# Kernel tuning notes

Hardware: AMD Instinct MI355X
Metric: run time of the kernel (lower is better)

Reference implementation:

```python
import jax, jax.numpy as jnp
import numpy as np

B, T, D, H = 2, 512, 512, 8
HD = D // H
FF = 4 * D
MOM_BETA, NOV_BETA, NOV_GAIN = 0.9, 0.95, 3.0
LR_MIN, LR_MAX, MAX_FW_NORM = 0.5, 3.0, 32.0


def setup_inputs() -> dict:
    key = jax.random.key(0)
    ks = jax.random.split(key, 10)
    s = 1.0 / np.sqrt(D)
    return {
        'x': jax.random.normal(ks[0], (B, T, D), jnp.float32),
        'Wq': jax.random.normal(ks[1], (D, D), jnp.float32) * s,
        'Wk1': jax.random.normal(ks[2], (D, D), jnp.float32) * s,
        'Wk2': jax.random.normal(ks[3], (D, D), jnp.float32) * s,
        'Wv': jax.random.normal(ks[4], (D, D), jnp.float32) * s,
        'Wo': jax.random.normal(ks[5], (D, D), jnp.float32) * s,
        'lambda_logit': jnp.zeros((H,), jnp.float32),  # sigmoid -> lambda_init = 0.5
        'ln1_g': jnp.ones((D,), jnp.float32), 'ln1_b': jnp.zeros((D,), jnp.float32),
        'base_weight': jax.random.normal(ks[6], (D, D), jnp.float32) * s,  # ~xavier
        'ttt_bias': jnp.zeros((D,), jnp.float32),
        'log_inner_lr': jnp.log(jnp.asarray(0.05, jnp.float32)),
        'ln2_g': jnp.ones((D,), jnp.float32), 'ln2_b': jnp.zeros((D,), jnp.float32),
        'W1': jax.random.normal(ks[7], (FF, D), jnp.float32) * s,
        'b1': jnp.zeros((FF,), jnp.float32),
        'W2': jax.random.normal(ks[8], (D, FF), jnp.float32) * (1.0 / np.sqrt(FF)),
        'b2': jnp.zeros((D,), jnp.float32),
        'ln3_g': jnp.ones((D,), jnp.float32), 'ln3_b': jnp.zeros((D,), jnp.float32),
    }


def _ln(x, g, b):
    m = x.mean(-1, keepdims=True)
    v = jnp.mean((x - m) ** 2, -1, keepdims=True)
    return (x - m) / jnp.sqrt(v + 1e-5) * g + b


def _diff_attn(x, Wq, Wk1, Wk2, Wv, Wo, lambda_logit):
    b, t, d = x.shape
    def heads(w):
        return jnp.einsum('btd,od->bto', x, w).reshape(b, t, H, HD).transpose(0, 2, 1, 3)
    q, k1, k2, v = heads(Wq), heads(Wk1), heads(Wk2), heads(Wv)
    scale = HD ** -0.5
    s1 = jnp.einsum('bhqd,bhkd->bhqk', q, k1) * scale
    s2 = jnp.einsum('bhqd,bhkd->bhqk', q, k2) * scale
    mask = jnp.tril(jnp.ones((t, t), bool))
    neg = jnp.finfo(s1.dtype).min
    s1 = jnp.where(mask, s1, neg)
    s2 = jnp.where(mask, s2, neg)
    lam = jax.nn.sigmoid(lambda_logit)[None, :, None, None]
    attn = jax.nn.softmax(s1, -1) - lam * jax.nn.softmax(s2, -1)
    attn = attn / jnp.clip(jnp.abs(attn).sum(-1, keepdims=True), 1e-6, None)
    o = jnp.einsum('bhqk,bhkd->bhqd', attn, v).transpose(0, 2, 1, 3).reshape(b, t, d)
    return jnp.einsum('btd,od->bto', o, Wo)


def _ttt(x, base_weight, ttt_bias, log_inner_lr):
    b = x.shape[0]
    inner_lr = jnp.clip(jnp.exp(log_inner_lr), 1e-5, 1.0)
    fw0 = jnp.broadcast_to(base_weight, (b, D, D)).astype(x.dtype) + 0.0
    mom0 = jnp.zeros_like(fw0)
    ema0 = jnp.zeros((b, D), x.dtype)
    lrm0 = jnp.ones((b, 1), x.dtype)

    def step(carry, x_t):  # x_t: [B, D]
        fw, mom, ema, lrm = carry
        y = jnp.einsum('bij,bj->bi', fw, x_t) + ttt_bias
        err = (y - x_t) / float(D)  # targets=None -> target is x_t
        g = jax.lax.stop_gradient(err[:, :, None] * x_t[:, None, :])  # first_order
        mom2 = MOM_BETA * mom + (1.0 - MOM_BETA) * g
        nov = jnp.abs(x_t - ema).mean(-1, keepdims=True)  # [B, 1]
        lr_scale = jnp.clip(1.0 + NOV_GAIN * nov, LR_MIN, LR_MAX)
        lrm2 = NOV_BETA * lrm + (1.0 - NOV_BETA) * lr_scale
        ema2 = NOV_BETA * ema + (1.0 - NOV_BETA) * x_t
        fw2 = fw - (inner_lr * lrm2)[:, :, None] * mom2
        norm = jnp.clip(jnp.sqrt((fw2 * fw2).sum((1, 2), keepdims=True)), 1e-6, None)
        fw2 = fw2 * jnp.minimum(MAX_FW_NORM / norm, 1.0)
        return (fw2, mom2, ema2, lrm2), y

    _, ys = jax.lax.scan(step, (fw0, mom0, ema0, lrm0), x.transpose(1, 0, 2))
    return ys.transpose(1, 0, 2)


def reference(x, Wq, Wk1, Wk2, Wv, Wo, lambda_logit, ln1_g, ln1_b, base_weight, ttt_bias, log_inner_lr, ln2_g, ln2_b, W1, b1, W2, b2, ln3_g, ln3_b):
    h = x + _diff_attn(_ln(x, ln1_g, ln1_b), Wq, Wk1, Wk2, Wv, Wo, lambda_logit)
    h = h + _ttt(_ln(h, ln2_g, ln2_b), base_weight, ttt_bias, log_inner_lr)
    z = _ln(h, ln3_g, ln3_b)
    z = jax.nn.gelu(jnp.einsum('btd,fd->btf', z, W1) + b1, approximate=False)
    h = h + jnp.einsum('btf,df->btd', z, W2) + b2
    return h
```

## Files before the change

kernel.cpp:

```cpp
#include <hip/hip_runtime.h>
#include <hip/hip_fp16.h>

typedef _Float16 f16;
typedef f16 f16x4 __attribute__((ext_vector_type(4)));
typedef f16 f16x8 __attribute__((ext_vector_type(8)));
typedef float f32x4 __attribute__((ext_vector_type(4)));

#define DEVI static __device__ __forceinline__

DEVI void gload_lds16(const void* g, void* l) {
  __builtin_amdgcn_global_load_lds(
      (const __attribute__((address_space(1))) unsigned int*)g,
      (__attribute__((address_space(3))) unsigned int*)l, 16, 0, 0);
}

DEVI float wave_red_sum64(float v) {
#pragma unroll
  for (int m = 1; m < 64; m <<= 1) v += __shfl_xor(v, m, 64);
  return v;
}
DEVI float wave_red_max64(float v) {
#pragma unroll
  for (int m = 1; m < 64; m <<= 1) v = fmaxf(v, __shfl_xor(v, m, 64));
  return v;
}

template <int CTRL>
DEVI float dpp_addf(float v) {
  int s = __builtin_amdgcn_update_dpp(0, __float_as_int(v), CTRL, 0xF, 0xF, true);
  return v + __int_as_float(s);
}
DEVI float redsum64(float v) {
  v = dpp_addf<0xB1>(v);
  v = dpp_addf<0x4E>(v);
  v = dpp_addf<0x141>(v);
  v = dpp_addf<0x140>(v);
  int t = __builtin_amdgcn_update_dpp(0, __float_as_int(v), 0x142, 0xA, 0xF, true);
  v += __int_as_float(t);
  t = __builtin_amdgcn_update_dpp(0, __float_as_int(v), 0x143, 0xC, 0xF, true);
  v += __int_as_float(t);
  return __int_as_float(__builtin_amdgcn_readlane(__float_as_int(v), 63));
}

__global__ void cvt_all_kernel(const float* __restrict__ s0, const float* __restrict__ s1,
                               const float* __restrict__ s2, const float* __restrict__ s3,
                               const float* __restrict__ s4, const float* __restrict__ s5,
                               const float* __restrict__ s6, f16* __restrict__ d,
                               const float* __restrict__ x, const float* __restrict__ ln1g,
                               const float* __restrict__ ln1b, f16* __restrict__ xlnH) {
  const int blk = blockIdx.x;
  if (blk >= 3328) {
    const int row = (blk - 3328) * 4 + ((int)threadIdx.x >> 6);
    const int lane = threadIdx.x & 63;
    const long base = (long)row * 512;
    const int c0 = lane * 4, c1 = 256 + lane * 4;
    float4 a0 = *(const float4*)(x + base + c0);
    float4 a1 = *(const float4*)(x + base + c1);
    float v[8] = {a0.x, a0.y, a0.z, a0.w, a1.x, a1.y, a1.z, a1.w};
    float s = 0.f;
#pragma unroll
    for (int k = 0; k < 8; k++) s += v[k];
    s = wave_red_sum64(s);
    const float mean = s * (1.f / 512.f);
    float vs = 0.f;
#pragma unroll
    for (int k = 0; k < 8; k++) { float dd = v[k] - mean; vs += dd * dd; }
    vs = wave_red_sum64(vs);
    const float rstd = rsqrtf(vs * (1.f / 512.f) + 1e-5f);
    float4 g0 = *(const float4*)(ln1g + c0), g1 = *(const float4*)(ln1g + c1);
    float4 p0 = *(const float4*)(ln1b + c0), p1 = *(const float4*)(ln1b + c1);
    const float gg[8] = {g0.x, g0.y, g0.z, g0.w, g1.x, g1.y, g1.z, g1.w};
    const float bv[8] = {p0.x, p0.y, p0.z, p0.w, p1.x, p1.y, p1.z, p1.w};
    float y[8];
#pragma unroll
    for (int k = 0; k < 8; k++) y[k] = (v[k] - mean) * rstd * gg[k] + bv[k];
    f16x4 o0 = {(f16)y[0], (f16)y[1], (f16)y[2], (f16)y[3]};
    f16x4 o1 = {(f16)y[4], (f16)y[5], (f16)y[6], (f16)y[7]};
    *(f16x4*)(xlnH + base + c0) = o0;
    *(f16x4*)(xlnH + base + c1) = o1;
    return;
  }
  const float* s; long dofs; int local;
  if (blk < 256)       { s = s0; dofs = 0;       local = blk; }
  else if (blk < 512)  { s = s1; dofs = 262144;  local = blk - 256; }
  else if (blk < 768)  { s = s2; dofs = 524288;  local = blk - 512; }
  else if (blk < 1024) { s = s3; dofs = 786432;  local = blk - 768; }
  else if (blk < 1280) { s = s4; dofs = 1048576; local = blk - 1024; }
  else if (blk < 2304) { s = s5; dofs = 1310720; local = blk - 1280; }
  else                 { s = s6; dofs = 2359296; local = blk - 2304; }
  const long i = (long)local * 1024 + threadIdx.x * 4;
  float4 v = *(const float4*)(s + i);
  f16x4 o = {(f16)v.x, (f16)v.y, (f16)v.z, (f16)v.w};
  *(f16x4*)(d + dofs + i) = o;
}

__global__ void ln_kernel(const float* __restrict__ in, const float* __restrict__ add,
                          const float* __restrict__ g, const float* __restrict__ b,
                          float* __restrict__ sumout, float* __restrict__ lnf,
                          f16* __restrict__ lnh) {
  const int row = blockIdx.x * 4 + (threadIdx.x >> 6);
  const int lane = threadIdx.x & 63;
  const long base = (long)row * 512;
  const int c0 = lane * 4, c1 = 256 + lane * 4;
  float4 a0 = *(const float4*)(in + base + c0);
  float4 a1 = *(const float4*)(in + base + c1);
  if (add) {
    float4 d0 = *(const float4*)(add + base + c0);
    float4 d1 = *(const float4*)(add + base + c1);
    a0.x += d0.x; a0.y += d0.y; a0.z += d0.z; a0.w += d0.w;
    a1.x += d1.x; a1.y += d1.y; a1.z += d1.z; a1.w += d1.w;
  }
  if (sumout) {
// ... 3 lines not shown
  float v[8] = {a0.x, a0.y, a0.z, a0.w, a1.x, a1.y, a1.z, a1.w};
  float s = 0.f;
#pragma unroll
  for (int k = 0; k < 8; k++) s += v[k];
  s = wave_red_sum64(s);
  const float mean = s * (1.f / 512.f);
  float vs = 0.f;
#pragma unroll
  for (int k = 0; k < 8; k++) { float d = v[k] - mean; vs += d * d; }
  vs = wave_red_sum64(vs);
  const float rstd = rsqrtf(vs * (1.f / 512.f) + 1e-5f);
  float4 g0 = *(const float4*)(g + c0), g1 = *(const float4*)(g + c1);
  float4 p0 = *(const float4*)(b + c0), p1 = *(const float4*)(b + c1);
  const float gg[8] = {g0.x, g0.y, g0.z, g0.w, g1.x, g1.y, g1.z, g1.w};
  const float bv[8] = {p0.x, p0.y, p0.z, p0.w, p1.x, p1.y, p1.z, p1.w};
  float y[8];
#pragma unroll
  for (int k = 0; k < 8; k++) y[k] = (v[k] - mean) * rstd * gg[k] + bv[k];
  if (lnf) {
    float4 o0 = {y[0], y[1], y[2], y[3]}, o1 = {y[4], y[5], y[6], y[7]};
    *(float4*)(lnf + base + c0) = o0;
    *(float4*)(lnf + base + c1) = o1;
  }
  if (lnh) {
    f16x4 o0 = {(f16)y[0], (f16)y[1], (f16)y[2], (f16)y[3]};
    f16x4 o1 = {(f16)y[4], (f16)y[5], (f16)y[6], (f16)y[7]};
    *(f16x4*)(lnh + base + c0) = o0;
    *(f16x4*)(lnh + base + c1) = o1;
  }
}

__global__ void red8ln_kernel(const float* __restrict__ parts, const float* __restrict__ xres,
                              const float* __restrict__ g, const float* __restrict__ b,
                              float* __restrict__ h1, float* __restrict__ x2out) {
  const int row = blockIdx.x * 4 + (threadIdx.x >> 6);
  const int lane = threadIdx.x & 63;
  const long base = (long)row * 512;
  const int c0 = lane * 4, c1 = 256 + lane * 4;
  float4 a0, a1;
  {
    float4 r = *(const float4*)(xres + base + c0);
    float sx = r.x, sy = r.y, sz = r.z, sw = r.w;
#pragma unroll
    for (int sl = 0; sl < 8; sl++) {
      float4 p = *(const float4*)(parts + (long)sl * 524288 + base + c0);
      sx += p.x; sy += p.y; sz += p.z; sw += p.w;
    }
    a0 = (float4){sx, sy, sz, sw};
  }
  {
    float4 r = *(const float4*)(xres + base + c1);
    float sx = r.x, sy = r.y, sz = r.z, sw = r.w;
#pragma unroll
    for (int sl = 0; sl < 8; sl++) {
      float4 p = *(const float4*)(parts + (long)sl * 524288 + base + c1);
      sx += p.x; sy += p.y; sz += p.z; sw += p.w;
    }
    a1 = (float4){sx, sy, sz, sw};
  }
  *(float4*)(h1 + base + c0) = a0;
  *(float4*)(h1 + base + c1) = a1;
  float v[8] = {a0.x, a0.y, a0.z, a0.w, a1.x, a1.y, a1.z, a1.w};
  float s = 0.f;
#pragma unroll
  for (int k = 0; k < 8; k++) s += v[k];
  s = wave_red_sum64(s);
  const float mean = s * (1.f / 512.f);
  float vs = 0.f;
#pragma unroll
  for (int k = 0; k < 8; k++) { float d = v[k] - mean; vs += d * d; }
  vs = wave_red_sum64(vs);
  const float rstd = rsqrtf(vs * (1.f / 512.f) + 1e-5f);
  float4 g0 = *(const float4*)(g + c0), g1 = *(const float4*)(g + c1);
  float4 p0 = *(const float4*)(b + c0), p1 = *(const float4*)(b + c1);
  const float gg[8] = {g0.x, g0.y, g0.z, g0.w, g1.x, g1.y, g1.z, g1.w};
  const float bv[8] = {p0.x, p0.y, p0.z, p0.w, p1.x, p1.y, p1.z, p1.w};
  float y[8];
#pragma unroll
  for (int k = 0; k < 8; k++) y[k] = (v[k] - mean) * rstd * gg[k] + bv[k];
  float4 o0 = {y[0], y[1], y[2], y[3]}, o1 = {y[4], y[5], y[6], y[7]};
  *(float4*)(x2out + base + c0) = o0;
  *(float4*)(x2out + base + c1) = o1;
}

enum { EPI_SCORES = 2, EPI_PV = 3, EPI_PART = 7, EPI_QKVPART = 8, EPI_GPART = 9 };

template <int EPI>
__launch_bounds__(256, 1) __global__
void gemm_bt(const f16* __restrict__ A, const f16* __restrict__ W, int lda, int ldw,
             long Az, long Wz, void* __restrict__ dst, const float* __restrict__ bias,
             const float* __restrict__ resid, int K, float scale, int zofs, int hcp) {
  if (EPI == EPI_SCORES && blockIdx.x > blockIdx.y) return;
  __shared__ f16 lA[128 * 64];
  __shared__ f16 lB[128 * 64];
  const int tid = threadIdx.x;
  const int wave = tid >> 6, lane = tid & 63;
  const int z = blockIdx.z;
  const f16* Ab;
  const f16* Wb;
  if (EPI == EPI_SCORES) {
    const int v_ = (z >= hcp) ? 1 : 0, head = z - v_ * hcp;
    Ab = A + (long)head * 32768 + (long)blockIdx.y * 128 * lda;
    Wb = W + (long)v_ * 524288 + (long)head * 32768 + (long)blockIdx.x * 128 * ldw;
  } else if (EPI == EPI_QKVPART) {
    const int widx = z & 3, ks = z >> 2;
    Ab = A + (long)blockIdx.y * 128 * lda + (long)ks * Az;
    Wb = W + (long)widx * Wz + (long)blockIdx.x * 128 * ldw + (long)ks * Az;
  } else {
    Ab = A + (long)z * Az + (long)blockIdx.y * 128 * lda;
    Wb = W + (long)z * Wz + (long)blockIdx.x * 128 * ldw;
  }

  f32x4 acc[4][4];
#pragma unroll
  for (int a = 0; a < 4; a++)
#pragma unroll
    for (int q = 0; q < 4; q++) acc[a][q] = (f32x4){0.f, 0.f, 0.f, 0.f};

// ... 30 lines not shown
      for (int nf = 0; nf < 4; nf++) {
        int r = wn + nf * 16 + (lane & 15);
        bfv[nf] = *(const f16x8*)((const char*)lB + r * 128 + (kb ^ ((r & 7) << 4)));
      }
#pragma unroll
      for (int mf = 0; mf < 4; mf++)
#pragma unroll
        for (int nf = 0; nf < 4; nf++)
          acc[mf][nf] = __builtin_amdgcn_mfma_f32_16x16x32_f16(af[mf], bfv[nf], acc[mf][nf], 0, 0, 0);
    }
  }

  const int wm = (wave >> 1) * 64, wn = (wave & 1) * 64;
  const int rbase = blockIdx.y * 128 + wm + ((lane >> 4) << 2);
  const int cbase = blockIdx.x * 128 + wn + (lane & 15);
#pragma unroll
  for (int mf = 0; mf < 4; mf++)
#pragma unroll
    for (int nf = 0; nf < 4; nf++)
#pragma unroll
      for (int j = 0; j < 4; j++) {
        const int m = rbase + mf * 16 + j;
        const int n = cbase + nf * 16;
        const float v = acc[mf][nf][j];
        if (EPI == EPI_SCORES) {
          ((float*)dst)[(long)z * 262144 + (long)m * 512 + n] = v * scale;
        } else if (EPI == EPI_PV) {
          if (n < 64) {
            const int hh = z + zofs;
            ((f16*)dst)[(long)((hh >> 3) * 512 + m) * 512 + (hh & 7) * 64 + n] = (f16)v;
          }
        } else if (EPI == EPI_GPART) {
          ((float*)dst)[(long)z * 2097152 + (long)m * 2048 + n] = v;
        } else {
          ((float*)dst)[(long)z * 524288 + (long)m * 512 + n] = v;
        }
      }
}

__global__ void qkv_red_kernel(const float* __restrict__ parts, f16* __restrict__ qkv) {
  const int idx = blockIdx.x * 256 + threadIdx.x;
  const int w = idx >> 17;
  const int r = idx & 131071;
  const int m = r >> 7;
  const int n4 = (r & 127) << 2;
  const float* p0 = parts + (long)w * 524288 + (long)m * 512 + n4;
  float4 a = *(const float4*)p0;
  float4 b = *(const float4*)(p0 + 4l * 524288);
  const float s0 = a.x + b.x, s1 = a.y + b.y, s2 = a.z + b.z, s3 = a.w + b.w;
  const int mb = (m >> 9) * 8 + (n4 >> 6);
  if (w < 3) {
    f16* d = qkv + (long)w * 524288;
    f16x4 o = {(f16)s0, (f16)s1, (f16)s2, (f16)s3};
    *(f16x4*)(d + (long)mb * 32768 + (m & 511) * 64 + (n4 & 63)) = o;
  } else {
    f16* d = qkv + 3l * 524288;
    const long bb = (long)mb * 32768 + (m & 511);
    d[bb + (long)(n4 & 63) * 512]       = (f16)s0;
    d[bb + (long)((n4 & 63) + 1) * 512] = (f16)s1;
    d[bb + (long)((n4 & 63) + 2) * 512] = (f16)s2;
    d[bb + (long)((n4 & 63) + 3) * 512] = (f16)s3;
  }
}

__global__ void red2gelu_kernel(const float* __restrict__ parts, const float* __restrict__ bias,
                                f16* __restrict__ zh) {
// ... 43 lines not shown
  float s1v[8] = {xa.x, xa.y, xa.z, xa.w, xb.x, xb.y, xb.z, xb.w};
  float s2v[8] = {ya.x, ya.y, ya.z, ya.w, yb.x, yb.y, yb.z, yb.w};
  int cols[8];
#pragma unroll
  for (int k = 0; k < 8; k++) cols[k] = (k < 4) ? (c0 + k) : (c1 + k - 4);
  float m1 = -3.0e38f, m2 = -3.0e38f;
#pragma unroll
  for (int k = 0; k < 8; k++)
    if (cols[k] <= i) { m1 = fmaxf(m1, s1v[k]); m2 = fmaxf(m2, s2v[k]); }
  m1 = wave_red_max64(m1);
  m2 = wave_red_max64(m2);
  float z1 = 0.f, z2 = 0.f, e1[8], e2[8];
#pragma unroll
  for (int k = 0; k < 8; k++) {
    const bool valid = cols[k] <= i;
    e1[k] = valid ? __expf(s1v[k] - m1) : 0.f;
    e2[k] = valid ? __expf(s2v[k] - m2) : 0.f;
    z1 += e1[k]; z2 += e2[k];
  }
  z1 = wave_red_sum64(z1);
  z2 = wave_red_sum64(z2);
  const float r1 = 1.f / z1, r2 = lam / z2;
  float p[8], l1 = 0.f;
#pragma unroll
  for (int k = 0; k < 8; k++) { p[k] = e1[k] * r1 - e2[k] * r2; l1 += fabsf(p[k]); }
  l1 = wave_red_sum64(l1);
  const float rn = 1.f / fmaxf(l1, 1e-6f);
  f16x4 o0 = {(f16)(p[0] * rn), (f16)(p[1] * rn), (f16)(p[2] * rn), (f16)(p[3] * rn)};
  f16x4 o1 = {(f16)(p[4] * rn), (f16)(p[5] * rn), (f16)(p[6] * rn), (f16)(p[7] * rn)};
  *(f16x4*)(attn + base + c0) = o0;
  *(f16x4*)(attn + base + c1) = o1;
}

#define ALD4(dst, p) asm volatile("global_load_dwordx4 %0, %1, off" : "=&v"(dst) : "v"(p) : "memory")
#define ALD1(dst, p) asm volatile("global_load_dword %0, %1, off" : "=&v"(dst) : "v"(p) : "memory")
#define VMWAIT(N)                                                             \
  {                                                                           \
    asm volatile("s_waitcnt vmcnt(" #N ")" ::: "memory");                     \
    __builtin_amdgcn_sched_barrier(0);                                        \
  }

#define EISSUE(X)                                                             \
  {                                                                           \
    ALD1(X[0], pe);        ALD1(X[1], pe + 512);                              \
    ALD1(X[2], pe + 1024); ALD1(X[3], pe + 1536);                             \
    ALD1(X[4], pe + 2048); ALD1(X[5], pe + 2560);                             \
    ALD1(X[6], pe + 3072); ALD1(X[7], pe + 3584);                             \
    pe += 4096;                                                               \
  }
#define ESTEP(V, T)                                                           \
  {                                                                           \
    dp[(long)(T) * 512] = fabsf((V) - ema);                                   \
    ema = fmaf(0.95f, ema, 0.05f * (V));                                      \
  }

__launch_bounds__(64, 1) __global__
void eta_diff_kernel(const float* __restrict__ x2, float* __restrict__ diff) {
  const int blk = blockIdx.x;
  const int b = blk >> 3;
  const int col = (blk & 7) * 64 + threadIdx.x;
  const float* pe = x2 + (long)b * 262144 + col;
  float* dp = diff + (long)b * 262144 + col;
  float ema = 0.f;
  float EA[8], EB[8];
  EISSUE(EA);
  EISSUE(EB);
  VMWAIT(8);
// ... 10 lines not shown
  }
  asm volatile("s_waitcnt vmcnt(0)" ::: "memory");
}

__global__ void eta_nov_kernel(const float* __restrict__ diff, float* __restrict__ nov,
                               int* __restrict__ flag) {
  if (blockIdx.x == 0 && threadIdx.x == 0) flag[0] = 0;
  const int row = blockIdx.x * 4 + (threadIdx.x >> 6);
  const int lane = threadIdx.x & 63;
  const float* dp = diff + (long)row * 512 + lane * 4;
  float4 a0 = *(const float4*)dp;
  float4 a1 = *(const float4*)(dp + 256);
  float s = ((a0.x + a0.y) + (a0.z + a0.w)) + ((a1.x + a1.y) + (a1.z + a1.w));
  s = wave_red_sum64(s);
  if (lane == 0) nov[row] = s * (1.f / 512.f);
}

__global__ void eta_scan_kernel(const float* __restrict__ nov, const float* __restrict__ loglr,
                                float* __restrict__ eta) {
  if (threadIdx.x != 0) return;
  const int b = blockIdx.x;
  float ilr = expf(loglr[0]);
  ilr = fminf(fmaxf(ilr, 1e-5f), 1.f);
  float lrm = 1.f;
  const float* pb = nov + (long)b * 512;
#pragma unroll 8
  for (int t = 0; t < 512; t++) {
    const float ls = fminf(fmaxf(fmaf(3.f, pb[t], 1.f), 0.5f), 3.f);
    lrm = fmaf(0.95f, lrm, 0.05f * ls);
    eta[b * 512 + t] = ilr * lrm;
  }
}

DEVI float dot8(const f32x4 F0, const f32x4 F1, const f32x4 X0, const f32x4 X1) {
  float a0 = F0.x * X0.x, a1 = F0.y * X0.y, a2 = F0.z * X0.z, a3 = F0.w * X0.w;
  a0 = fmaf(F1.x, X1.x, a0); a1 = fmaf(F1.y, X1.y, a1);
  a2 = fmaf(F1.z, X1.z, a2); a3 = fmaf(F1.w, X1.w, a3);
  return (a0 + a1) + (a2 + a3);
}
DEVI void upd8(f32x4& M0, f32x4& M1, f32x4& F0, f32x4& F1, float c1, float e,
               const f32x4 X0, const f32x4 X1, float& ns) {
  M0.x = fmaf(0.9f, M0.x, c1 * X0.x); F0.x = fmaf(-e, M0.x, F0.x); ns = fmaf(F0.x, F0.x, ns);
  M0.y = fmaf(0.9f, M0.y, c1 * X0.y); F0.y = fmaf(-e, M0.y, F0.y); ns = fmaf(F0.y, F0.y, ns);
  M0.z = fmaf(0.9f, M0.z, c1 * X0.z); F0.z = fmaf(-e, M0.z, F0.z); ns = fmaf(F0.z, F0.z, ns);
  M0.w = fmaf(0.9f, M0.w, c1 * X0.w); F0.w = fmaf(-e, M0.w, F0.w); ns = fmaf(F0.w, F0.w, ns);
  M1.x = fmaf(0.9f, M1.x, c1 * X1.x); F1.x = fmaf(-e, M1.x, F1.x); ns = fmaf(F1.x, F1.x, ns);
  M1.y = fmaf(0.9f, M1.y, c1 * X1.y); F1.y = fmaf(-e, M1.y, F1.y); ns = fmaf(F1.y, F1.y, ns);
  M1.z = fmaf(0.9f, M1.z, c1 * X1.z); F1.z = fmaf(-e, M1.z, F1.z); ns = fmaf(F1.z, F1.z, ns);
  M1.w = fmaf(0.9f, M1.w, c1 * X1.w); F1.w = fmaf(-e, M1.w, F1.w); ns = fmaf(F1.w, F1.w, ns);
}

#define TISSUE2(X, RA, RB, ET)                                                \
  {                                                                           \
    ALD4(X[0], pxc);        ALD4(X[1], pxc + 4);                              \
    ALD4(X[2], pxc + 512);  ALD4(X[3], pxc + 516);                            \
    ALD4(X[4], pxc + 1024); ALD4(X[5], pxc + 1028);                           \
    ALD4(X[6], pxc + 1536); ALD4(X[7], pxc + 1540);                           \
    ALD1(RA[0], pxra);        ALD1(RA[1], pxra + 512);                        \
    ALD1(RA[2], pxra + 1024); ALD1(RA[3], pxra + 1536);                       \
    ALD1(RB[0], pxrb);        ALD1(RB[1], pxrb + 512);                        \
    ALD1(RB[2], pxrb + 1024); ALD1(RB[3], pxrb + 1536);                       \
    ALD4(ET, per);                                                            \
    pxc += 2048; pxra += 2048; pxrb += 2048; per += 4;                        \
  }

#define TSTEP2(X0v, X1v, rAv, rBv, ev, K)                                     \
  {                                                                           \
    const float pA_ = redsum64(dot8(fA0, fA1, X0v, X1v));                     \
    const float pB_ = redsum64(dot8(fB0, fB1, X0v, X1v));                     \
    const float yA_ = pA_ + biasA, yB_ = pB_ + biasB;                         \
    ysA[K] = yA_; ysB[K] = yB_;                                               \
    const float c1A_ = (yA_ - (rAv)) * (0.1f / 512.f);                        \
    const float c1B_ = (yB_ - (rBv)) * (0.1f / 512.f);                        \
    const float e_ = (ev);                                                    \
    float ns_ = 0.f;                                                          \
    upd8(mA0, mA1, fA0, fA1, c1A_, e_, X0v, X1v, ns_);                        \
    upd8(mB0, mB1, fB0, fB1, c1B_, e_, X0v, X1v, ns_);                        \
    nsmax = fmaxf(nsmax, ns_);                                                \
  }

__launch_bounds__(64, 1) __global__
void ttt_fast_kernel(const float* __restrict__ x2, const float* __restrict__ base_w,
                     const float* __restrict__ tbias, const float* __restrict__ eta,
                     float* __restrict__ yT, float* __restrict__ npB) {
  const int blk = blockIdx.x;
  const int b = blk >> 8;
  const int rA = blk & 255;
  const int lane = threadIdx.x;
  const float* xb = x2 + (long)b * 262144;

  f32x4 fA0, fA1, fB0, fB1;
  float biasA, biasB;
  ALD4(fA0, base_w + (long)rA * 512 + lane * 8);
  ALD4(fA1, base_w + (long)rA * 512 + lane * 8 + 4);
  ALD4(fB0, base_w + (long)(rA + 256) * 512 + lane * 8);
  ALD4(fB1, base_w + (long)(rA + 256) * 512 + lane * 8 + 4);
  ALD1(biasA, tbias + rA);
  ALD1(biasB, tbias + rA + 256);

  f32x4 mA0 = {0.f, 0.f, 0.f, 0.f}, mA1 = mA0, mB0 = mA0, mB1 = mA0;
  float ysA[8], ysB[8];
  float nsmax = 0.f;

  const float* pxc = xb + lane * 8;
  const float* pxra = xb + rA;
  const float* pxrb = xb + rA + 256;
  const float* per = eta + b * 512;
  float* pyA = yT + (long)(b * 512 + rA) * 512;
  float* pyB = yT + (long)(b * 512 + rA + 256) * 512;

  f32x4 XA[8], XB[8], EA, EB;
  float RA0[4], RB0[4], RA1[4], RB1[4];
  TISSUE2(XA, RA0, RB0, EA);
  TISSUE2(XB, RA1, RB1, EB);
  VMWAIT(17);

#pragma unroll 1
  for (int T = 0; T < 512; T += 8) {
    TSTEP2(XA[0], XA[1], RA0[0], RB0[0], EA.x, 0);
    TSTEP2(XA[2], XA[3], RA0[1], RB0[1], EA.y, 1);
    TSTEP2(XA[4], XA[5], RA0[2], RB0[2], EA.z, 2);
    TSTEP2(XA[6], XA[7], RA0[3], RB0[3], EA.w, 3);
    TISSUE2(XA, RA0, RB0, EA);
    VMWAIT(17);
    TSTEP2(XB[0], XB[1], RA1[0], RB1[0], EB.x, 4);
    TSTEP2(XB[2], XB[3], RA1[1], RB1[1], EB.y, 5);
    TSTEP2(XB[4], XB[5], RA1[2], RB1[2], EB.z, 6);
    TSTEP2(XB[6], XB[7], RA1[3], RB1[3], EB.w, 7);
    if (lane == 0) {
      *(float4*)(pyA + T)     = (float4){ysA[0], ysA[1], ysA[2], ysA[3]};
      *(float4*)(pyA + T + 4) = (float4){ysA[4], ysA[5], ysA[6], ysA[7]};
      *(float4*)(pyB + T)     = (float4){ysB[0], ysB[1], ysB[2], ysB[3]};
      *(float4*)(pyB + T + 4) = (float4){ysB[4], ysB[5], ysB[6], ysB[7]};
    }
    TISSUE2(XB, RA1, RB1, EB);
    VMWAIT(21);
  }
  asm volatile("s_waitcnt vmcnt(0)" ::: "memory");
  const float tot = redsum64(nsmax);
  if (lane == 0) npB[blk] = tot;
}

__global__ void transpose2v_kernel(const float* __restrict__ yT, float* __restrict__ ysb,
                                   const float* __restrict__ npB, int* __restrict__ flag) {
  const int s = blockIdx.z;
  if (s == 2) {
    if (blockIdx.x != 0 || blockIdx.y != 0) return;
    const int tid = threadIdx.x;
    const int wave = tid >> 6, lane = tid & 63;
    float a = npB[tid];
    float c = npB[tid + 256];
    a = wave_red_sum64(a);
    c = wave_red_sum64(c);
    __shared__ float pa[4], pc[4];
    if (lane == 0) { pa[wave] = a; pc[wave] = c; }
    __syncthreads();
    if (tid == 0) {
      const float s0 = (pa[0] + pa[1]) + (pa[2] + pa[3]);
      const float s1 = (pc[0] + pc[1]) + (pc[2] + pc[3]);
      if (s0 > 1000.f || s1 > 1000.f) atomicOr(flag, 1);
    }
    return;
  }
  __shared__ float tile[64][65];
  const float* src = yT + (long)s * 262144;
  float* dst = ysb + (long)s * 262144;
  const int ti = blockIdx.y, tj = blockIdx.x;
  const int tr = threadIdx.x >> 4;
  const int tc = (threadIdx.x & 15) * 4;
#pragma unroll
  for (int p = 0; p < 4; p++) {
    const int r = tr + p * 16;
    float4 v = *(const float4*)(src + (long)(ti * 64 + r) * 512 + tj * 64 + tc);
    tile[r][tc] = v.x; tile[r][tc + 1] = v.y; tile[r][tc + 2] = v.z; tile[r][tc + 3] = v.w;
  }
  __syncthreads();
#pragma unroll
  for (int p = 0; p < 4; p++) {
    const int j = tr + p * 16;
    float4 v = {tile[tc][j], tile[tc + 1][j], tile[tc + 2][j], tile[tc + 3][j]};
    *(float4*)(dst + (long)(tj * 64 + j) * 512 + ti * 64 + tc) = v;
  }
}

__launch_bounds__(1024, 1) __global__
void ttt_fallback_kernel(const int* __restrict__ flag, const float* __restrict__ x2,
                         const float* __restrict__ base_w, const float* __restrict__ tbias,
                         const float* __restrict__ eta, float* __restrict__ ys,
                         float* __restrict__ fwg, float* __restrict__ momg) {
  if (flag[0] == 0) return;
  const int b = blockIdx.x;
  const int tid = threadIdx.x;
  const int wave = tid >> 6, lane = tid & 63;
  float* fw = fwg + (long)b * 262144;
  float* mm = momg + (long)b * 262144;
  for (int e = tid; e < 262144; e += 1024) { fw[e] = base_w[e]; mm[e] = 0.f; }
  __shared__ float xs[512], errs[512], red[16];
  const float* xb = x2 + (long)b * 262144;
  for (int t = 0; t < 512; t++) {
    __syncthreads();
    if (tid < 512) xs[tid] = xb[t * 512 + tid];
    __syncthreads();
    if (tid < 512) {
      float acc = 0.f;
      for (int c = 0; c < 512; c++) acc = fmaf(fw[(long)tid * 512 + c], xs[c], acc);
      const float y = acc + tbias[tid];
      ys[((long)b * 512 + t) * 512 + tid] = y;
      errs[tid] = (y - xs[tid]) * (1.f / 512.f);
    }
    __syncthreads();
    const float eta_t = eta[b * 512 + t];
    float nsq = 0.f;
    for (int e = tid; e < 262144; e += 1024) {
      const int r = e >> 9, c = e & 511;
      const float m2 = fmaf(0.9f, mm[e], 0.1f * errs[r] * xs[c]);
// ... 38 lines not shown
  const float* ln2b   = (const float*)d_in[13];
  const float* W1     = (const float*)d_in[14];
  const float* b1     = (const float*)d_in[15];
  const float* W2     = (const float*)d_in[16];
  const float* b2     = (const float*)d_in[17];
  const float* ln3g   = (const float*)d_in[18];
  const float* ln3b   = (const float*)d_in[19];
  float* out = (float*)d_out;

  char* ws = (char*)d_ws;
  size_t off = 0;
  auto alloc = [&](size_t bytes) {
    size_t o = off;
    off += (bytes + 255) & ~(size_t)255;
    return o;
  };
  f16* WqH   = (f16*)(ws + alloc(262144 * 2));
  f16* Wk1H  = (f16*)(ws + alloc(262144 * 2));
  f16* Wk2H  = (f16*)(ws + alloc(262144 * 2));
  f16* WvH   = (f16*)(ws + alloc(262144 * 2));
  f16* WoH   = (f16*)(ws + alloc(262144 * 2));
  f16* W1H   = (f16*)(ws + alloc(1048576 * 2));
  f16* W2H   = (f16*)(ws + alloc(1048576 * 2));
  (void)Wk1H; (void)Wk2H; (void)WvH; (void)W1H;
  f16* xlnH  = (f16*)(ws + alloc(524288 * 2));
  f16* qh    = (f16*)(ws + alloc(524288 * 2));
  f16* k1h   = (f16*)(ws + alloc(524288 * 2));
  f16* k2h   = (f16*)(ws + alloc(524288 * 2));
  f16* vTh   = (f16*)(ws + alloc(524288 * 2));
  (void)k2h;
  f16* obtd  = (f16*)(ws + alloc(524288 * 2));
  f16* x3h   = (f16*)(ws + alloc(524288 * 2));
  f16* zh    = (f16*)(ws + alloc(2097152 * 2));
  float* h1  = (float*)(ws + alloc(524288 * 4));
  float* x2  = (float*)(ws + alloc(524288 * 4));
  float* ysb = (float*)(ws + alloc(524288 * 4));
  float* h2  = (float*)(ws + alloc(524288 * 4));
  float* eta = (float*)(ws + alloc(1024 * 4));
  float* npB = (float*)(ws + alloc(512 * 4));
  float* nov = (float*)(ws + alloc(1024 * 4));
  int* flag  = (int*)(ws + alloc(256));
  float* parts16 = (float*)(ws + alloc((size_t)16 * 1024 * 1024));
  float* yT    = parts16;
  float* nvd   = parts16 + 524288;
  float* fwfb  = parts16 + 1048576;
  float* momfb = parts16 + 1572864;

  int hc = 16;
  while (hc > 1 && off + (size_t)hc * (262144ull * 4 * 2 + 262144ull * 2) > ws_size) hc >>= 1;
  float* S1  = (float*)(ws + alloc((size_t)hc * 262144 * 4));
  float* S2  = (float*)(ws + alloc((size_t)hc * 262144 * 4));
  f16* attnb = (f16*)(ws + alloc((size_t)hc * 262144 * 2));
  (void)S2;

  cvt_all_kernel<<<3584, 256, 0, stream>>>(Wq, Wk1, Wk2, Wv, Wo, W1, W2, WqH,
                                           x, ln1g, ln1b, xlnH);

  gemm_bt<EPI_QKVPART><<<dim3(4, 8, 8), 256, 0, stream>>>(
      xlnH, WqH, 512, 512, 256, 262144, parts16, nullptr, nullptr, 256, 1.f, 0, 0);
  qkv_red_kernel<<<2048, 256, 0, stream>>>(parts16, qh);

  const int nc = 16 / hc;
  for (int c = 0; c < nc; c++) {
    const int cs = c * hc;
    gemm_bt<EPI_SCORES><<<dim3(4, 4, 2 * hc), 256, 0, stream>>>(
        qh + (long)cs * 32768, k1h + (long)cs * 32768, 64, 64, 0, 0, S1,
        nullptr, nullptr, 64, 0.125f, 0, hc);
    softmax_diff_kernel<<<hc * 128, 256, 0, stream>>>(S1, S2, lamlog, attnb, cs);
    gemm_bt<EPI_PV><<<dim3(1, 4, hc), 256, 0, stream>>>(
        attnb, vTh + (long)cs * 32768, 512, 512, 262144, 32768, obtd,
        nullptr, nullptr, 512, 1.f, cs, 0);
  }

  gemm_bt<EPI_PART><<<dim3(4, 8, 8), 256, 0, stream>>>(
      obtd, WoH, 512, 512, 64, 64, parts16, nullptr, nullptr, 64, 1.f, 0, 0);
  red8ln_kernel<<<256, 256, 0, stream>>>(parts16, x, ln2g, ln2b, h1, x2);

  eta_diff_kernel<<<16, 64, 0, stream>>>(x2, nvd);
  eta_nov_kernel<<<256, 256, 0, stream>>>(nvd, nov, flag);
  eta_scan_kernel<<<2, 64, 0, stream>>>(nov, loglr, eta);
  ttt_fast_kernel<<<512, 64, 0, stream>>>(x2, basew, tttb, eta, yT, npB);
  transpose2v_kernel<<<dim3(8, 8, 3), 256, 0, stream>>>(yT, ysb, npB, flag);
  ttt_fallback_kernel<<<2, 1024, 0, stream>>>(flag, x2, basew, tttb, eta, ysb, fwfb, momfb);

  ln_kernel<<<256, 256, 0, stream>>>(h1, ysb, ln3g, ln3b, h2, nullptr, x3h);

  gemm_bt<EPI_GPART><<<dim3(16, 8, 2), 256, 0, stream>>>(
      x3h, W1H, 512, 512, 256, 256, parts16, nullptr, nullptr, 256, 1.f, 0, 0);
  red2gelu_kernel<<<2048, 256, 0, stream>>>(parts16, b1, zh);
  gemm_bt<EPI_PART><<<dim3(4, 8, 8), 256, 0, stream>>>(
      zh, W2H, 2048, 2048, 256, 256, parts16, nullptr, nullptr, 256, 1.f, 0, 0);
  red8_kernel<<<512, 256, 0, stream>>>(parts16, h2, b2, out);
}
```

Measured before the change: 273.3 us.

## Replace sequential TTT scan with Gram-matrix triangular solve formulation

Drops the per-token sequential fast-weight recurrence kernel. In its place, the TTT outputs are rewritten algebraically: x2·base_weightᵀ and the Gram matrix x2·x2ᵀ come from fp16 GEMMs, a per-batch table of momentum-weighted learning rates is built, and a blocked lower-triangular solve recovers the per-token errors. The fast-weight norm check is rebuilt from further GEMMs and reductions, and the original fallback kernel still runs when the norm clip would trigger. Long serial dependency chains become mostly matrix work. The price is fp16 rounding in the Gram and error terms and a solve kernel that runs on only 16 blocks.

```diff
diff --git a/kernel.cpp b/kernel.cpp
--- a/kernel.cpp
+++ b/kernel.cpp
@@ -25,32 +25,16 @@
   return v;
 }
 
-template <int CTRL>
-DEVI float dpp_addf(float v) {
-  int s = __builtin_amdgcn_update_dpp(0, __float_as_int(v), CTRL, 0xF, 0xF, true);
-  return v + __int_as_float(s);
-}
-DEVI float redsum64(float v) {
-  v = dpp_addf<0xB1>(v);
-  v = dpp_addf<0x4E>(v);
-  v = dpp_addf<0x141>(v);
-  v = dpp_addf<0x140>(v);
-  int t = __builtin_amdgcn_update_dpp(0, __float_as_int(v), 0x142, 0xA, 0xF, true);
-  v += __int_as_float(t);
-  t = __builtin_amdgcn_update_dpp(0, __float_as_int(v), 0x143, 0xC, 0xF, true);
-  v += __int_as_float(t);
-  return __int_as_float(__builtin_amdgcn_readlane(__float_as_int(v), 63));
-}
-
 __global__ void cvt_all_kernel(const float* __restrict__ s0, const float* __restrict__ s1,
                                const float* __restrict__ s2, const float* __restrict__ s3,
                                const float* __restrict__ s4, const float* __restrict__ s5,
                                const float* __restrict__ s6, f16* __restrict__ d,
+                               const float* __restrict__ bw, f16* __restrict__ bwh,
                                const float* __restrict__ x, const float* __restrict__ ln1g,
                                const float* __restrict__ ln1b, f16* __restrict__ xlnH) {
   const int blk = blockIdx.x;
-  if (blk >= 3328) {
-    const int row = (blk - 3328) * 4 + ((int)threadIdx.x >> 6);
+  if (blk >= 3584) {
+    const int row = (blk - 3584) * 4 + ((int)threadIdx.x >> 6);
     const int lane = threadIdx.x & 63;
     const long base = (long)row * 512;
     const int c0 = lane * 4, c1 = 256 + lane * 4;
@@ -78,6 +62,13 @@
     f16x4 o1 = {(f16)y[4], (f16)y[5], (f16)y[6], (f16)y[7]};
     *(f16x4*)(xlnH + base + c0) = o0;
     *(f16x4*)(xlnH + base + c1) = o1;
+    return;
+  }
+  if (blk >= 3328) {
+    const long i = (long)(blk - 3328) * 1024 + threadIdx.x * 4;
+    float4 v = *(const float4*)(bw + i);
+    f16x4 o = {(f16)v.x, (f16)v.y, (f16)v.z, (f16)v.w};
+    *(f16x4*)(bwh + i) = o;
     return;
   }
   const float* s; long dofs; int local;
@@ -147,7 +138,8 @@
 
 __global__ void red8ln_kernel(const float* __restrict__ parts, const float* __restrict__ xres,
                               const float* __restrict__ g, const float* __restrict__ b,
-                              float* __restrict__ h1, float* __restrict__ x2out) {
+                              float* __restrict__ h1, float* __restrict__ x2out,
+                              f16* __restrict__ x2h) {
   const int row = blockIdx.x * 4 + (threadIdx.x >> 6);
   const int lane = threadIdx.x & 63;
   const long base = (long)row * 512;
@@ -196,9 +188,14 @@
   float4 o0 = {y[0], y[1], y[2], y[3]}, o1 = {y[4], y[5], y[6], y[7]};
   *(float4*)(x2out + base + c0) = o0;
   *(float4*)(x2out + base + c1) = o1;
-}
-
-enum { EPI_SCORES = 2, EPI_PV = 3, EPI_PART = 7, EPI_QKVPART = 8, EPI_GPART = 9 };
+  f16x4 h0 = {(f16)y[0], (f16)y[1], (f16)y[2], (f16)y[3]};
+  f16x4 hh1 = {(f16)y[4], (f16)y[5], (f16)y[6], (f16)y[7]};
+  *(f16x4*)(x2h + base + c0) = h0;
+  *(f16x4*)(x2h + base + c1) = hh1;
+}
+
+enum { EPI_SCORES = 2, EPI_PV = 3, EPI_PART = 7, EPI_QKVPART = 8, EPI_GPART = 9,
+       EPI_GRAM = 10, EPI_MXG = 11 };
 
 template <int EPI>
 __launch_bounds__(256, 1) __global__
@@ -295,6 +292,11 @@
           }
         } else if (EPI == EPI_GPART) {
           ((float*)dst)[(long)z * 2097152 + (long)m * 2048 + n] = v;
+        } else if (EPI == EPI_GRAM) {
+          ((float*)dst)[(long)z * 262144 + (long)m * 512 + n] = v * scale;
+        } else if (EPI == EPI_MXG) {
+          const long ii = (long)z * 262144 + (long)m * 512 + n;
+          ((f16*)dst)[ii] = (f16)(v * resid[ii] * (1.f / 262144.f));
         } else {
           ((float*)dst)[(long)z * 524288 + (long)m * 512 + n] = v;
         }
@@ -404,7 +406,6 @@
   *(f16x4*)(attn + base + c1) = o1;
 }
 
-#define ALD4(dst, p) asm volatile("global_load_dwordx4 %0, %1, off" : "=&v"(dst) : "v"(p) : "memory")
 #define ALD1(dst, p) asm volatile("global_load_dword %0, %1, off" : "=&v"(dst) : "v"(p) : "memory")
 #define VMWAIT(N)                                                             \
   {                                                                           \
@@ -481,155 +482,153 @@
   }
 }
 
-DEVI float dot8(const f32x4 F0, const f32x4 F1, const f32x4 X0, const f32x4 X1) {
-  float a0 = F0.x * X0.x, a1 = F0.y * X0.y, a2 = F0.z * X0.z, a3 = F0.w * X0.w;
-  a0 = fmaf(F1.x, X1.x, a0); a1 = fmaf(F1.y, X1.y, a1);
-  a2 = fmaf(F1.z, X1.z, a2); a3 = fmaf(F1.w, X1.w, a3);
-  return (a0 + a1) + (a2 + a3);
-}
-DEVI void upd8(f32x4& M0, f32x4& M1, f32x4& F0, f32x4& F1, float c1, float e,
-               const f32x4 X0, const f32x4 X1, float& ns) {
-  M0.x = fmaf(0.9f, M0.x, c1 * X0.x); F0.x = fmaf(-e, M0.x, F0.x); ns = fmaf(F0.x, F0.x, ns);
-  M0.y = fmaf(0.9f, M0.y, c1 * X0.y); F0.y = fmaf(-e, M0.y, F0.y); ns = fmaf(F0.y, F0.y, ns);
-  M0.z = fmaf(0.9f, M0.z, c1 * X0.z); F0.z = fmaf(-e, M0.z, F0.z); ns = fmaf(F0.z, F0.z, ns);
-  M0.w = fmaf(0.9f, M0.w, c1 * X0.w); F0.w = fmaf(-e, M0.w, F0.w); ns = fmaf(F0.w, F0.w, ns);
-  M1.x = fmaf(0.9f, M1.x, c1 * X1.x); F1.x = fmaf(-e, M1.x, F1.x); ns = fmaf(F1.x, F1.x, ns);
-  M1.y = fmaf(0.9f, M1.y, c1 * X1.y); F1.y = fmaf(-e, M1.y, F1.y); ns = fmaf(F1.y, F1.y, ns);
-  M1.z = fmaf(0.9f, M1.z, c1 * X1.z); F1.z = fmaf(-e, M1.z, F1.z); ns = fmaf(F1.z, F1.z, ns);
-  M1.w = fmaf(0.9f, M1.w, c1 * X1.w); F1.w = fmaf(-e, M1.w, F1.w); ns = fmaf(F1.w, F1.w, ns);
-}
-
-#define TISSUE2(X, RA, RB, ET)                                                \
-  {                                                                           \
-    ALD4(X[0], pxc);        ALD4(X[1], pxc + 4);                              \
-    ALD4(X[2], pxc + 512);  ALD4(X[3], pxc + 516);                            \
-    ALD4(X[4], pxc + 1024); ALD4(X[5], pxc + 1028);                           \
-    ALD4(X[6], pxc + 1536); ALD4(X[7], pxc + 1540);                           \
-    ALD1(RA[0], pxra);        ALD1(RA[1], pxra + 512);                        \
-    ALD1(RA[2], pxra + 1024); ALD1(RA[3], pxra + 1536);                       \
-    ALD1(RB[0], pxrb);        ALD1(RB[1], pxrb + 512);                        \
-    ALD1(RB[2], pxrb + 1024); ALD1(RB[3], pxrb + 1536);                       \
-    ALD4(ET, per);                                                            \
-    pxc += 2048; pxra += 2048; pxrb += 2048; per += 4;                        \
-  }
-
-#define TSTEP2(X0v, X1v, rAv, rBv, ev, K)                                     \
-  {                                                                           \
-    const float pA_ = redsum64(dot8(fA0, fA1, X0v, X1v));                     \
-    const float pB_ = redsum64(dot8(fB0, fB1, X0v, X1v));                     \
-    const float yA_ = pA_ + biasA, yB_ = pB_ + biasB;                         \
-    ysA[K] = yA_; ysB[K] = yB_;                                               \
-    const float c1A_ = (yA_ - (rAv)) * (0.1f / 512.f);                        \
-    const float c1B_ = (yB_ - (rBv)) * (0.1f / 512.f);                        \
-    const float e_ = (ev);                                                    \
-    float ns_ = 0.f;                                                          \
-    upd8(mA0, mA1, fA0, fA1, c1A_, e_, X0v, X1v, ns_);                        \
-    upd8(mB0, mB1, fB0, fB1, c1B_, e_, X0v, X1v, ns_);                        \
-    nsmax = fmaxf(nsmax, ns_);                                                \
-  }
-
-__launch_bounds__(64, 1) __global__
-void ttt_fast_kernel(const float* __restrict__ x2, const float* __restrict__ base_w,
-                     const float* __restrict__ tbias, const float* __restrict__ eta,
-                     float* __restrict__ yT, float* __restrict__ npB) {
-  const int blk = blockIdx.x;
-  const int b = blk >> 8;
-  const int rA = blk & 255;
-  const int lane = threadIdx.x;
-  const float* xb = x2 + (long)b * 262144;
-
-  f32x4 fA0, fA1, fB0, fB1;
-  float biasA, biasB;
-  ALD4(fA0, base_w + (long)rA * 512 + lane * 8);
-  ALD4(fA1, base_w + (long)rA * 512 + lane * 8 + 4);
-  ALD4(fB0, base_w + (long)(rA + 256) * 512 + lane * 8);
-  ALD4(fB1, base_w + (long)(rA + 256) * 512 + lane * 8 + 4);
-  ALD1(biasA, tbias + rA);
-  ALD1(biasB, tbias + rA + 256);
-
-  f32x4 mA0 = {0.f, 0.f, 0.f, 0.f}, mA1 = mA0, mB0 = mA0, mB1 = mA0;
-  float ysA[8], ysB[8];
-  float nsmax = 0.f;
-
-  const float* pxc = xb + lane * 8;
-  const float* pxra = xb + rA;
-  const float* pxrb = xb + rA + 256;
-  const float* per = eta + b * 512;
-  float* pyA = yT + (long)(b * 512 + rA) * 512;
-  float* pyB = yT + (long)(b * 512 + rA + 256) * 512;
-
-  f32x4 XA[8], XB[8], EA, EB;
-  float RA0[4], RB0[4], RA1[4], RB1[4];
-  TISSUE2(XA, RA0, RB0, EA);
-  TISSUE2(XB, RA1, RB1, EB);
-  VMWAIT(17);
-
-#pragma unroll 1
-  for (int T = 0; T < 512; T += 8) {
-    TSTEP2(XA[0], XA[1], RA0[0], RB0[0], EA.x, 0);
-    TSTEP2(XA[2], XA[3], RA0[1], RB0[1], EA.y, 1);
-    TSTEP2(XA[4], XA[5], RA0[2], RB0[2], EA.z, 2);
-    TSTEP2(XA[6], XA[7], RA0[3], RB0[3], EA.w, 3);
-    TISSUE2(XA, RA0, RB0, EA);
-    VMWAIT(17);
-    TSTEP2(XB[0], XB[1], RA1[0], RB1[0], EB.x, 4);
-    TSTEP2(XB[2], XB[3], RA1[1], RB1[1], EB.y, 5);
-    TSTEP2(XB[4], XB[5], RA1[2], RB1[2], EB.z, 6);
-    TSTEP2(XB[6], XB[7], RA1[3], RB1[3], EB.w, 7);
-    if (lane == 0) {
-      *(float4*)(pyA + T)     = (float4){ysA[0], ysA[1], ysA[2], ysA[3]};
-      *(float4*)(pyA + T + 4) = (float4){ysA[4], ysA[5], ysA[6], ysA[7]};
-      *(float4*)(pyB + T)     = (float4){ysB[0], ysB[1], ysB[2], ysB[3]};
-      *(float4*)(pyB + T + 4) = (float4){ysB[4], ysB[5], ysB[6], ysB[7]};
-    }
-    TISSUE2(XB, RA1, RB1, EB);
-    VMWAIT(21);
-  }
-  asm volatile("s_waitcnt vmcnt(0)" ::: "memory");
-  const float tot = redsum64(nsmax);
-  if (lane == 0) npB[blk] = tot;
-}
-
-__global__ void transpose2v_kernel(const float* __restrict__ yT, float* __restrict__ ysb,
-                                   const float* __restrict__ npB, int* __restrict__ flag) {
-  const int s = blockIdx.z;
-  if (s == 2) {
-    if (blockIdx.x != 0 || blockIdx.y != 0) return;
-    const int tid = threadIdx.x;
-    const int wave = tid >> 6, lane = tid & 63;
-    float a = npB[tid];
-    float c = npB[tid + 256];
-    a = wave_red_sum64(a);
-    c = wave_red_sum64(c);
-    __shared__ float pa[4], pc[4];
-    if (lane == 0) { pa[wave] = a; pc[wave] = c; }
-    __syncthreads();
-    if (tid == 0) {
-      const float s0 = (pa[0] + pa[1]) + (pa[2] + pa[3]);
-      const float s1 = (pc[0] + pc[1]) + (pc[2] + pc[3]);
-      if (s0 > 1000.f || s1 > 1000.f) atomicOr(flag, 1);
-    }
+__global__ void wtab_kernel(const float* __restrict__ eta, const float* __restrict__ basew,
+                            float* __restrict__ wUT32, f16* __restrict__ wUT16,
+                            float* __restrict__ fwn2) {
+  if (blockIdx.x == 2) {
+    __shared__ float part[512];
+    float s = 0.f;
+    for (int e = threadIdx.x; e < 262144; e += 512) { float v = basew[e]; s = fmaf(v, v, s); }
+    part[threadIdx.x] = s;
+    __syncthreads();
+    for (int st = 256; st > 0; st >>= 1) {
+      if ((int)threadIdx.x < st) part[threadIdx.x] += part[threadIdx.x + st];
+      __syncthreads();
+    }
+    if (threadIdx.x == 0) fwn2[0] = part[0];
     return;
   }
-  __shared__ float tile[64][65];
-  const float* src = yT + (long)s * 262144;
-  float* dst = ysb + (long)s * 262144;
-  const int ti = blockIdx.y, tj = blockIdx.x;
-  const int tr = threadIdx.x >> 4;
-  const int tc = (threadIdx.x & 15) * 4;
-#pragma unroll
-  for (int p = 0; p < 4; p++) {
-    const int r = tr + p * 16;
-    float4 v = *(const float4*)(src + (long)(ti * 64 + r) * 512 + tj * 64 + tc);
-    tile[r][tc] = v.x; tile[r][tc + 1] = v.y; tile[r][tc + 2] = v.z; tile[r][tc + 3] = v.w;
-  }
-  __syncthreads();
-#pragma unroll
-  for (int p = 0; p < 4; p++) {
-    const int j = tr + p * 16;
-    float4 v = {tile[tc][j], tile[tc + 1][j], tile[tc + 2][j], tile[tc + 3][j]};
-    *(float4*)(dst + (long)(tj * 64 + j) * 512 + ti * 64 + tc) = v;
-  }
+  const int b = blockIdx.x, u = threadIdx.x;
+  const float* et = eta + b * 512;
+  float* w32 = wUT32 + (long)b * 262144;
+  f16* w16 = wUT16 + (long)b * 262144;
+  float q = 0.1f, wv = 0.f;
+  for (int t = 0; t < 512; t++) {
+    if (t < u) {
+      w32[(long)t * 512 + u] = 0.f;
+      w16[(long)t * 512 + u] = (f16)0.f;
+    } else {
+      wv = fmaf(q, et[t], wv);
+      q *= 0.9f;
+      w32[(long)t * 512 + u] = wv;
+      w16[(long)t * 512 + u] = (f16)wv;
+    }
+  }
+}
+
+__global__ void e0_kernel(const float* __restrict__ Y0, const float* __restrict__ x2,
+                          const float* __restrict__ tttb, float* __restrict__ e0) {
+  const long i = ((long)blockIdx.x * 256 + threadIdx.x) * 4;
+  float4 y = *(const float4*)(Y0 + i);
+  float4 x = *(const float4*)(x2 + i);
+  float4 bb = *(const float4*)(tttb + (int)(i & 511));
+  float4 o = {(y.x + bb.x - x.x) * (1.f / 512.f), (y.y + bb.y - x.y) * (1.f / 512.f),
+              (y.z + bb.z - x.z) * (1.f / 512.f), (y.w + bb.w - x.w) * (1.f / 512.f)};
+  *(float4*)(e0 + i) = o;
+}
+
+__global__ void solve_kernel(const float* __restrict__ e0, const float* __restrict__ wUT32,
+                             const float* __restrict__ G, const float* __restrict__ x2,
+                             float* __restrict__ E, f16* __restrict__ Eh,
+                             float* __restrict__ ysb) {
+  extern __shared__ char smem[];
+  f16* Elds = (f16*)smem;
+  float* Ls = (float*)(smem + 65536);
+  float* Rhs = (float*)(smem + 65536 + 16384);
+  const int b = blockIdx.z, g = blockIdx.x;
+  const int tid = threadIdx.x, w = tid >> 6, l = tid & 63;
+  const int c = g * 64 + l;
+  const float* e0b = e0 + (long)b * 262144;
+  const float* wb = wUT32 + (long)b * 262144;
+  const float* Gb = G + (long)b * 262144;
+  const float* x2b = x2 + (long)b * 262144;
+  float* Eb = E + (long)b * 262144;
+  f16* Ehb = Eh + (long)b * 262144;
+  float* ysp = ysb + (long)b * 262144;
+
+  for (int i = 0; i < 8; i++) {
+    const int t0 = i * 64;
+    float acc[8];
+#pragma unroll
+    for (int r = 0; r < 8; r++) acc[r] = e0b[(long)(t0 + w * 8 + r) * 512 + c];
+    for (int j = 0; j < i; j++) {
+      __syncthreads();
+      for (int e = tid; e < 4096; e += 512) {
+        const int tp = e >> 6, up = e & 63;
+        Ls[e] = wb[(long)(t0 + tp - 1) * 512 + j * 64 + up] *
+                Gb[(long)(t0 + tp) * 512 + j * 64 + up] * (1.f / 512.f);
+      }
+      __syncthreads();
+      for (int up = 0; up < 64; up++) {
+        const float ev = (float)Elds[(j * 64 + up) * 64 + l];
+#pragma unroll
+        for (int r = 0; r < 8; r++)
+          acc[r] = fmaf(-Ls[(w * 8 + r) * 64 + up], ev, acc[r]);
+      }
+    }
+    __syncthreads();
+#pragma unroll
+    for (int r = 0; r < 8; r++) Rhs[(w * 8 + r) * 64 + l] = acc[r];
+    for (int e = tid; e < 4096; e += 512) {
+      const int tp = e >> 6, up = e & 63;
+      if (up < tp)
+        Ls[e] = wb[(long)(t0 + tp - 1) * 512 + i * 64 + up] *
+                Gb[(long)(t0 + tp) * 512 + i * 64 + up] * (1.f / 512.f);
+    }
+    __syncthreads();
+    if (w == 0) {
+      float ech[64];
+#pragma unroll
+      for (int tp = 0; tp < 64; tp++) {
+        float v = Rhs[tp * 64 + l];
+#pragma unroll
+        for (int up = 0; up < tp; up++)
+          v = fmaf(-Ls[tp * 64 + up], ech[up], v);
+        ech[tp] = v;
+        Elds[(t0 + tp) * 64 + l] = (f16)v;
+      }
+#pragma unroll
+      for (int tp = 0; tp < 64; tp++) {
+        const long gi = (long)(t0 + tp) * 512 + c;
+        const float v = ech[tp];
+        Eb[gi] = v;
+        Ehb[gi] = (f16)(512.f * v);
+        ysp[gi] = fmaf(512.f, v, x2b[gi]);
+      }
+    }
+    __syncthreads();
+  }
+}
+
+__global__ void a_kernel(const float* __restrict__ E, const float* __restrict__ Y0,
+                         float* __restrict__ a) {
+  const int row = blockIdx.x * 4 + (threadIdx.x >> 6);
+  const int lane = threadIdx.x & 63;
+  const float* ep = E + (long)row * 512 + lane * 4;
+  const float* yp = Y0 + (long)row * 512 + lane * 4;
+  float4 e0v = *(const float4*)ep, y0 = *(const float4*)yp;
+  float4 e1 = *(const float4*)(ep + 256), y1 = *(const float4*)(yp + 256);
+  float s = ((e0v.x * y0.x + e0v.y * y0.y) + (e0v.z * y0.z + e0v.w * y0.w)) +
+            ((e1.x * y1.x + e1.y * y1.y) + (e1.z * y1.z + e1.w * y1.w));
+  s = wave_red_sum64(s);
+  if (lane == 0) a[row] = s;
+}
+
+__global__ void normt_kernel(const float* __restrict__ wUT32, const float* __restrict__ V,
+                             const float* __restrict__ a, const float* __restrict__ fwn2,
+                             int* __restrict__ flag) {
+  const int b = blockIdx.x, t = threadIdx.x;
+  const float* wrow = wUT32 + (long)b * 262144 + (long)t * 512;
+  const float* ab = a + b * 512;
+  const float* Vb = V + (long)b * 262144;
+  float s1 = 0.f, s2 = 0.f;
+  for (int u = 0; u <= t; u++) {
+    const float wv = wrow[u];
+    s1 = fmaf(wv, ab[u], s1);
+    s2 = fmaf(wv, Vb[(long)u * 512 + t], s2);
+  }
+  const float n2 = fwn2[0] - 2.f * s1 + s2;
+  if (n2 > 1000.f) atomicOr(flag, 1);
 }
 
 __launch_bounds__(1024, 1) __global__
@@ -734,19 +733,30 @@
   f16* obtd  = (f16*)(ws + alloc(524288 * 2));
   f16* x3h   = (f16*)(ws + alloc(524288 * 2));
   f16* zh    = (f16*)(ws + alloc(2097152 * 2));
+  f16* x2h   = (f16*)(ws + alloc(524288 * 2));
+  f16* bwh   = (f16*)(ws + alloc(262144 * 2));
   float* h1  = (float*)(ws + alloc(524288 * 4));
   float* x2  = (float*)(ws + alloc(524288 * 4));
   float* ysb = (float*)(ws + alloc(524288 * 4));
   float* h2  = (float*)(ws + alloc(524288 * 4));
   float* eta = (float*)(ws + alloc(1024 * 4));
-  float* npB = (float*)(ws + alloc(512 * 4));
   float* nov = (float*)(ws + alloc(1024 * 4));
   int* flag  = (int*)(ws + alloc(256));
   float* parts16 = (float*)(ws + alloc((size_t)16 * 1024 * 1024));
-  float* yT    = parts16;
-  float* nvd   = parts16 + 524288;
-  float* fwfb  = parts16 + 1048576;
-  float* momfb = parts16 + 1572864;
+  float* Y0    = parts16;
+  float* Gg    = parts16 + 524288;
+  float* wUT32 = parts16 + 1048576;
+  float* e0b   = parts16 + 1572864;
+  float* Ebuf  = parts16 + 2097152;
+  float* nvd   = parts16 + 2621440;
+  float* Vb    = nvd;
+  f16* wUT16   = (f16*)(parts16 + 3145728);
+  f16* Ehb     = (f16*)(parts16 + 3407872);
+  f16* Mxh     = (f16*)(parts16 + 3670016);
+  float* ab    = parts16 + 3932160;
+  float* fwn2  = parts16 + 3933184;
+  float* fwfb  = Y0;
+  float* momfb = Gg;
 
   int hc = 16;
   while (hc > 1 && off + (size_t)hc * (262144ull * 4 * 2 + 262144ull * 2) > ws_size) hc >>= 1;
@@ -755,8 +765,8 @@
   f16* attnb = (f16*)(ws + alloc((size_t)hc * 262144 * 2));
   (void)S2;
 
-  cvt_all_kernel<<<3584, 256, 0, stream>>>(Wq, Wk1, Wk2, Wv, Wo, W1, W2, WqH,
-                                           x, ln1g, ln1b, xlnH);
+  cvt_all_kernel<<<3840, 256, 0, stream>>>(Wq, Wk1, Wk2, Wv, Wo, W1, W2, WqH,
+                                           basew, bwh, x, ln1g, ln1b, xlnH);
 
   gemm_bt<EPI_QKVPART><<<dim3(4, 8, 8), 256, 0, stream>>>(
       xlnH, WqH, 512, 512, 256, 262144, parts16, nullptr, nullptr, 256, 1.f, 0, 0);
@@ -776,13 +786,24 @@
 
   gemm_bt<EPI_PART><<<dim3(4, 8, 8), 256, 0, stream>>>(
       obtd, WoH, 512, 512, 64, 64, parts16, nullptr, nullptr, 64, 1.f, 0, 0);
-  red8ln_kernel<<<256, 256, 0, stream>>>(parts16, x, ln2g, ln2b, h1, x2);
-
+  red8ln_kernel<<<256, 256, 0, stream>>>(parts16, x, ln2g, ln2b, h1, x2, x2h);
+
+  gemm_bt<EPI_GRAM><<<dim3(4, 4, 2), 256, 0, stream>>>(
+      x2h, bwh, 512, 512, 262144, 0, Y0, nullptr, nullptr, 512, 1.f, 0, 0);
+  gemm_bt<EPI_GRAM><<<dim3(4, 4, 2), 256, 0, stream>>>(
+      x2h, x2h, 512, 512, 262144, 262144, Gg, nullptr, nullptr, 512, 1.f, 0, 0);
   eta_diff_kernel<<<16, 64, 0, stream>>>(x2, nvd);
   eta_nov_kernel<<<256, 256, 0, stream>>>(nvd, nov, flag);
   eta_scan_kernel<<<2, 64, 0, stream>>>(nov, loglr, eta);
-  ttt_fast_kernel<<<512, 64, 0, stream>>>(x2, basew, tttb, eta, yT, npB);
-  transpose2v_kernel<<<dim3(8, 8, 3), 256, 0, stream>>>(yT, ysb, npB, flag);
+  wtab_kernel<<<3, 512, 0, stream>>>(eta, basew, wUT32, wUT16, fwn2);
+  e0_kernel<<<512, 256, 0, stream>>>(Y0, x2, tttb, e0b);
+  solve_kernel<<<dim3(8, 1, 2), 512, 98304, stream>>>(e0b, wUT32, Gg, x2, Ebuf, Ehb, ysb);
+  gemm_bt<EPI_MXG><<<dim3(4, 4, 2), 256, 0, stream>>>(
+      Ehb, Ehb, 512, 512, 262144, 262144, Mxh, nullptr, Gg, 512, 1.f, 0, 0);
+  gemm_bt<EPI_GRAM><<<dim3(4, 4, 2), 256, 0, stream>>>(
+      Mxh, wUT16, 512, 512, 262144, 262144, Vb, nullptr, nullptr, 512, 1.f, 0, 0);
+  a_kernel<<<256, 256, 0, stream>>>(Ebuf, Y0, ab);
+  normt_kernel<<<2, 512, 0, stream>>>(wUT32, Vb, ab, fwn2, flag);
   ttt_fallback_kernel<<<2, 1024, 0, stream>>>(flag, x2, basew, tttb, eta, ysb, fwfb, momfb);
 
   ln_kernel<<<256, 256, 0, stream>>>(h1, ysb, ln3g, ln3b, h2, nullptr, x3h);
```

Measured after the change: 949.7 us. +247.5%, slower.
